# Performance work log

Measured on AMD Instinct MI355X. Metric: run time of the kernel, lower is better.

Reference implementation:

```python
import jax, jax.numpy as jnp
import numpy as np

B, C, H, W = 8, 96, 224, 224
WS, SS, NH = 7, 3, 3          # window size, shift size, num heads
HD = C // NH                  # head dim = 32
N = WS * WS                   # tokens per window = 49
MLP_H = 4 * C
EPS = 1e-5


def _rel_pos_index():
    coords = np.stack(np.meshgrid(np.arange(WS), np.arange(WS), indexing='ij'))  # (2, ws, ws)
    cf = coords.reshape(2, -1)                       # (2, N)
    rel = cf[:, :, None] - cf[:, None, :]            # (2, N, N)
    rel = rel.transpose(1, 2, 0).copy()              # (N, N, 2)
    rel[:, :, 0] += WS - 1
    rel[:, :, 1] += WS - 1
    rel[:, :, 0] *= 2 * WS - 1
    return rel.sum(-1)                               # (N, N) int


def _attn_mask():
    # Swin shifted-window mask: (num_windows, N, N) with 0 / -100
    img = np.zeros((H, W), np.float32)
    cnt = 0
    for hs in (slice(0, -WS), slice(-WS, -SS), slice(-SS, None)):
        for ws_ in (slice(0, -WS), slice(-WS, -SS), slice(-SS, None)):
            img[hs, ws_] = cnt
            cnt += 1
    mw = img.reshape(H // WS, WS, W // WS, WS).transpose(0, 2, 1, 3).reshape(-1, N)
    m = mw[:, None, :] - mw[:, :, None]
    return np.where(m != 0, np.float32(-100.0), np.float32(0.0))


def setup_inputs() -> dict:
    key = jax.random.key(0)
    ks = jax.random.split(key, 8)
    s = 0.02
    return {
        "x": jax.random.normal(ks[0], (B, C, H, W), jnp.float32),
        "attn_mask": jnp.asarray(_attn_mask()),
        "norm1_g": jnp.ones((C,), jnp.float32),
        "norm1_b": jnp.zeros((C,), jnp.float32),
        "qkv_w": jax.random.normal(ks[1], (C, 3 * C), jnp.float32) * s,
        "qkv_b": jnp.zeros((3 * C,), jnp.float32),
        "rpb": jax.random.normal(ks[2], ((2 * WS - 1) ** 2, NH), jnp.float32) * s,
        "proj_w": jax.random.normal(ks[3], (C, C), jnp.float32) * s,
        "proj_b": jnp.zeros((C,), jnp.float32),
        "norm2_g": jnp.ones((C,), jnp.float32),
        "norm2_b": jnp.zeros((C,), jnp.float32),
        "fc1_w": jax.random.normal(ks[4], (C, MLP_H), jnp.float32) * s,
        "fc1_b": jnp.zeros((MLP_H,), jnp.float32),
        "fc2_w": jax.random.normal(ks[5], (MLP_H, C), jnp.float32) * s,
        "fc2_b": jnp.zeros((C,), jnp.float32),
    }


def _ln(x, g, b):
    mu = jnp.mean(x, axis=-1, keepdims=True)
    var = jnp.var(x, axis=-1, keepdims=True)
    return (x - mu) * jax.lax.rsqrt(var + EPS) * g + b


def reference(x, attn_mask, norm1_g, norm1_b, qkv_w, qkv_b, rpb, proj_w, proj_b,
              norm2_g, norm2_b, fc1_w, fc1_b, fc2_w, fc2_b):
    shortcut = x
    # (B,C,H,W) -> (B,HW,C) -> LN -> (B,H,W,C)
    xl = jnp.transpose(x, (0, 2, 3, 1)).reshape(B, H * W, C)
    xl = _ln(xl, norm1_g, norm1_b).reshape(B, H, W, C)
    # H,W divisible by WS: pad_r = pad_b = 0
    sx = jnp.roll(xl, (-SS, -SS), axis=(1, 2))
    # window partition -> (B*nW, N, C)
    xw = sx.reshape(B, H // WS, WS, W // WS, WS, C).transpose(0, 1, 3, 2, 4, 5).reshape(-1, N, C)
    B_ = xw.shape[0]
    nW = B_ // B
    qkv = (xw @ qkv_w + qkv_b).reshape(B_, N, 3, NH, HD).transpose(2, 0, 3, 1, 4)
    q = qkv[0] * (HD ** -0.5)
    k, v = qkv[1], qkv[2]
    attn = jnp.einsum('bhnd,bhmd->bhnm', q, k)           # (B_, NH, N, N)
    rel_idx = jnp.asarray(_rel_pos_index())
    bias = rpb[rel_idx.reshape(-1)].reshape(N, N, NH).transpose(2, 0, 1)  # (NH, N, N)
    attn = attn + bias[None]
    attn = attn.reshape(B, nW, NH, N, N) + attn_mask[None, :, None]
    attn = jax.nn.softmax(attn.reshape(B_, NH, N, N), axis=-1)
    out = jnp.einsum('bhnm,bhmd->bhnd', attn, v).transpose(0, 2, 1, 3).reshape(B_, N, C)
    out = out @ proj_w + proj_b
    # window reverse -> (B, H, W, C)
    out = out.reshape(B, H // WS, W // WS, WS, WS, C).transpose(0, 1, 3, 2, 4, 5).reshape(B, H, W, C)
    out = jnp.roll(out, (SS, SS), axis=(1, 2))
    # faithful to original: permute(0,1,3,2) then raw reshape to (B,C,H,W)
    out = jnp.transpose(out, (0, 1, 3, 2)).reshape(B, C, H, W)
    x1 = shortcut + out
    # MLP branch, faithful: permute(0,1,3,2) then raw reshape to (B,HW,C)
    xm = jnp.transpose(x1, (0, 1, 3, 2)).reshape(B, H * W, C)
    xm = _ln(xm, norm2_g, norm2_b)
    xm = jax.nn.gelu(xm @ fc1_w + fc1_b, approximate=False) @ fc2_w + fc2_b
    xm = xm.reshape(B, C, H, W)
    return x1 + xm
```

## Files before the change

kernel.cpp:

```cpp
#include <hip/hip_runtime.h>
#include <hip/hip_bf16.h>


typedef __attribute__((ext_vector_type(4))) float f32x4;
typedef __attribute__((ext_vector_type(8))) short s16x8;

constexpr int B_ = 8;
constexpr int M_ = 96 * 224 * 224;

__device__ __forceinline__ ushort f2bs(float f) {
    __hip_bfloat16 h = __float2bfloat16(f);
    ushort u; __builtin_memcpy(&u, &h, 2); return u;
}
__device__ __forceinline__ float bs2f(ushort u) {
    __hip_bfloat16 h; __builtin_memcpy(&h, &u, 2); return __bfloat162float(h);
}
__device__ __forceinline__ f32x4 mfma16(s16x8 a, s16x8 b, f32x4 c) {
    return __builtin_amdgcn_mfma_f32_16x16x32_bf16(a, b, c, 0, 0, 0);
}
__device__ __forceinline__ float gelu_f(float v) {
    float s  = v * 0.70710678118654752f;
    float as = fabsf(s);
    float t  = __builtin_amdgcn_rcpf(fmaf(0.3275911f, as, 1.0f));
    float p  = fmaf(fmaf(fmaf(fmaf(1.061405429f, t, -1.453152027f), t,
                   1.421413741f), t, -0.284496736f), t, 0.254829592f) * t;
    float y  = 1.0f - p * __expf(-s * s);
    float er = copysignf(y, s);
    return 0.5f * v * (1.0f + er);
}

__global__ __launch_bounds__(256) void prep_kernel(
    const float* __restrict__ qkvw, const float* __restrict__ projw,
    const float* __restrict__ w1,   const float* __restrict__ w2,
    ushort* __restrict__ wq, ushort* __restrict__ wp,
    ushort* __restrict__ wf1, ushort* __restrict__ wf2)
{
    int i = blockIdx.x * 256 + threadIdx.x;
    if (i < 27648) { int n = i / 96, k = i % 96;  wq[i]  = f2bs(qkvw[k * 288 + n]); }
    if (i < 9216)  { int n = i / 96, k = i % 96;  wp[i]  = f2bs(projw[k * 96 + n]); }
    if (i < 36864) {
        int n = i / 96,  k = i % 96;   wf1[i] = f2bs(w1[k * 384 + n]);
        int n2 = i / 384, k2 = i % 384; wf2[i] = f2bs(w2[k2 * 96 + n2]);
    }
}

__global__ __launch_bounds__(256) void attn_kernel(
    const float* __restrict__ x,
    const float* __restrict__ amask,
    const float* __restrict__ n1g, const float* __restrict__ n1b,
    const float* __restrict__ qkvb,
    const float* __restrict__ rpb,
    const float* __restrict__ projb,
    const ushort* __restrict__ wq, const ushort* __restrict__ wp,
    ushort* __restrict__ x1)
{
    __shared__ __align__(16) ushort T[64][104];
    __shared__ __align__(16) ushort K[64][104];
    __shared__ __align__(16) ushort vT[96][72];
    __shared__ __align__(16) ushort Pws[4][16][72];
    __shared__ float rpbs[512];

    const int tid  = threadIdx.x;
    const int wave = tid >> 6, lane = tid & 63;
    const int cu   = lane & 15;
    const int g4   = lane >> 4;
    const int gk8  = g4 << 3;
    const int gr4  = g4 << 2;

    const int blk = (blockIdx.x & 7) * 1024 + (blockIdx.x >> 3);
    const int b   = blk >> 10;
    const int wi  = blk & 1023;
    const int wh  = wi >> 5, ww = wi & 31;
    const int bM  = b * M_;
    const bool need_mask = (wh == 31) || (ww == 31);

    for (int i = tid; i < 507; i += 256) rpbs[i] = rpb[i];

    const int t49 = tid % 49;
    const int g5  = tid / 49;
    int hh_s = 0, wc_s = 0;
    if (tid < 245) {
        int i = t49 / 7, j = t49 % 7;
        hh_s = wh * 7 + i + 3; if (hh_s >= 224) hh_s -= 224;
        wc_s = ww * 7 + j + 3; if (wc_s >= 224) wc_s -= 224;
    }

    if (tid < 245) {
        const float* xp = x + bM + g5 * 50176 + hh_s * 224 + wc_s;
        ushort* dT = &T[t49][g5];
        for (int c = g5; c < 96; c += 5) {
            *dT = f2bs(*xp);
            xp += 5 * 50176; dT += 5;
        }
    }
    {
        uint* z = (uint*)&T[49][0];
        for (int i = tid; i < 780; i += 256) z[i] = 0u;
    }
    __syncthreads();

    if (tid < 196) {
        int t = tid >> 2, s = tid & 3;
        float sum = 0.f, sq = 0.f;
        float vv[24];
        #pragma unroll
        for (int i = 0; i < 24; ++i) {
            vv[i] = bs2f(T[t][s * 24 + i]);
            sum += vv[i]; sq += vv[i] * vv[i];
        }
        sum += __shfl_xor(sum, 1); sq += __shfl_xor(sq, 1);
        sum += __shfl_xor(sum, 2); sq += __shfl_xor(sq, 2);
        float mu   = sum * (1.0f / 96.0f);
        float rstd = rsqrtf(sq * (1.0f / 96.0f) - mu * mu + 1e-5f);
        #pragma unroll
        for (int i = 0; i < 24; ++i) {
            int c = s * 24 + i;
            T[t][c] = f2bs((vv[i] - mu) * rstd * n1g[c] + n1b[c]);
        }
    }
    __syncthreads();

    const int ar = (wave << 4) | cu;
    const int tr = (wave << 4) + gr4;

    {
        s16x8 a0 = *(const s16x8*)&T[ar][gk8];
        s16x8 a1 = *(const s16x8*)&T[ar][32 + gk8];
        s16x8 a2 = *(const s16x8*)&T[ar][64 + gk8];
        f32x4 qreg[6];
        #pragma unroll
        for (int nt = 0; nt < 18; ++nt) {
            int nc = (nt << 4) | cu;
            const ushort* bp = wq + nc * 96 + gk8;
            s16x8 b0 = *(const s16x8*)(bp);
            s16x8 b1 = *(const s16x8*)(bp + 32);
            s16x8 b2 = *(const s16x8*)(bp + 64);
            f32x4 acc = {0.f, 0.f, 0.f, 0.f};
            acc = mfma16(a0, b0, acc);
            acc = mfma16(a1, b1, acc);
            acc = mfma16(a2, b2, acc);
            float bias = qkvb[nc];
            if (nt < 6) {
                #pragma unroll
                for (int r = 0; r < 4; ++r)
                    qreg[nt][r] = (acc[r] + bias) * 0.17677669529663689f;
            } else if (nc < 192) {
                #pragma unroll
                for (int r = 0; r < 4; ++r) K[tr + r][nc - 96] = f2bs(acc[r] + bias);
            } else {
                int d = nc - 192;
                ushort4 pk;
                pk.x = f2bs(acc[0] + bias); pk.y = f2bs(acc[1] + bias);
                pk.z = f2bs(acc[2] + bias); pk.w = f2bs(acc[3] + bias);
                *(ushort4*)&vT[d][tr] = pk;
            }
        }
        #pragma unroll
        for (int qn = 0; qn < 6; ++qn)
            #pragma unroll
            for (int r = 0; r < 4; ++r)
                T[tr + r][(qn << 4) | cu] = f2bs(qreg[qn][r]);
    }
    __syncthreads();

    int u7d[4], u7m[4];
    #pragma unroll
    for (int ut = 0; ut < 4; ++ut) {
        int u = (ut << 4) | cu;
        u7d[ut] = u / 7; u7m[ut] = u % 7;
    }
    s16x8 ones8;
    #pragma unroll
    for (int i = 0; i < 8; ++i) ones8[i] = (short)0x3F80;

    #pragma unroll
    for (int it = 0; it < 3; ++it) {
        const int hh = it;
        const int t0r = tr;

        s16x8 aq = *(const s16x8*)&T[ar][(hh << 5) + gk8];
        f32x4 sa[4];
        #pragma unroll
        for (int ut = 0; ut < 4; ++ut) {
            s16x8 bk = *(const s16x8*)&K[(ut << 4) | cu][(hh << 5) + gk8];
            f32x4 z = {0.f, 0.f, 0.f, 0.f};
            sa[ut] = mfma16(aq, bk, z);
        }
        #pragma unroll
        for (int ut = 0; ut < 4; ++ut) {
            int u = (ut << 4) | cu;
            #pragma unroll
            for (int r = 0; r < 4; ++r) {
                int t = t0r + r;
                float s = sa[ut][r];
                if (t < 49 && u < 49) {
                    int dr = t / 7 - u7d[ut] + 6, dc = t % 7 - u7m[ut] + 6;
                    s += rpbs[(dr * 13 + dc) * 3 + hh];
                    if (need_mask) s += amask[(wi * 49 + t) * 49 + u];
                } else if (u >= 49) {
                    s = -1e30f;
                }
                sa[ut][r] = s;
            }
        }
        #pragma unroll
        for (int r = 0; r < 4; ++r) {
            float m = fmaxf(fmaxf(sa[0][r], sa[1][r]), fmaxf(sa[2][r], sa[3][r]));
            m = fmaxf(m, __shfl_xor(m, 1)); m = fmaxf(m, __shfl_xor(m, 2));
            m = fmaxf(m, __shfl_xor(m, 4)); m = fmaxf(m, __shfl_xor(m, 8));
            sa[0][r] = __expf(sa[0][r] - m);
            sa[1][r] = __expf(sa[1][r] - m);
            sa[2][r] = __expf(sa[2][r] - m);
            sa[3][r] = __expf(sa[3][r] - m);
        }
        #pragma unroll
        for (int ut = 0; ut < 4; ++ut) {
            int u = (ut << 4) | cu;
            #pragma unroll
            for (int r = 0; r < 4; ++r) Pws[wave][gr4 + r][u] = f2bs(sa[ut][r]);
        }
        s16x8 pa0 = *(const s16x8*)&Pws[wave][cu][gk8];
        s16x8 pa1 = *(const s16x8*)&Pws[wave][cu][32 + gk8];
        f32x4 accd = {0.f, 0.f, 0.f, 0.f};
        accd = mfma16(pa0, ones8, accd);
        accd = mfma16(pa1, ones8, accd);
        f32x4 acco[2];
        #pragma unroll
        for (int nt = 0; nt < 2; ++nt) {
            int d = (hh << 5) + (nt << 4) + cu;
            s16x8 bv0 = *(const s16x8*)&vT[d][gk8];
            s16x8 bv1 = *(const s16x8*)&vT[d][32 + gk8];
            f32x4 acc = {0.f, 0.f, 0.f, 0.f};
            acc = mfma16(pa0, bv0, acc);
            acc = mfma16(pa1, bv1, acc);
            acco[nt] = acc;
        }
        float inv[4];
        #pragma unroll
        for (int r = 0; r < 4; ++r) inv[r] = __builtin_amdgcn_rcpf(accd[r]);
        #pragma unroll
        for (int nt = 0; nt < 2; ++nt)
            #pragma unroll
            for (int r = 0; r < 4; ++r)
                T[t0r + r][(hh << 5) + (nt << 4) + cu] = f2bs(acco[nt][r] * inv[r]);
    }

    {
        s16x8 a0 = *(const s16x8*)&T[ar][gk8];
        s16x8 a1 = *(const s16x8*)&T[ar][32 + gk8];
        s16x8 a2 = *(const s16x8*)&T[ar][64 + gk8];
        #pragma unroll
        for (int nt = 0; nt < 6; ++nt) {
            int nc = (nt << 4) | cu;
            const ushort* bp = wp + nc * 96 + gk8;
            s16x8 b0 = *(const s16x8*)(bp);
            s16x8 b1 = *(const s16x8*)(bp + 32);
            s16x8 b2 = *(const s16x8*)(bp + 64);
            f32x4 acc = {0.f, 0.f, 0.f, 0.f};
            acc = mfma16(a0, b0, acc);
            acc = mfma16(a1, b1, acc);
            acc = mfma16(a2, b2, acc);
            float bias = projb[nc];
            #pragma unroll
            for (int r = 0; r < 4; ++r) T[tr + r][nc] = f2bs(acc[r] + bias);
        }
    }
    __syncthreads();

    if (tid < 245) {
        const int base = bM + (hh_s * 96 + g5) * 224 + wc_s;
        const float* xp = x + base;
        ushort* dx = x1 + base;
        const ushort* Tp = &T[t49][g5];
        for (int c = g5; c < 96; c += 5) {
            *dx = f2bs(*xp + bs2f(*Tp));
            xp += 5 * 224; dx += 5 * 224; Tp += 5;
        }
    }
}

__global__ __launch_bounds__(256) void transpose_kernel(
    const ushort* __restrict__ x1, ushort* __restrict__ x1p)
{
    __shared__ ushort tile[32][36];
    const int id      = blockIdx.x;
    const int tile_id = id % 49;
    const int slab    = id / 49;
    const int h0 = (tile_id / 7) * 32;
    const int w0 = (tile_id % 7) * 32;
    const ushort* src = x1  + slab * 50176;
    ushort*       dst = x1p + slab * 50176;

    const int i = threadIdx.x >> 3;
    const int j = (threadIdx.x & 7) * 4;

    *(ushort4*)&tile[i][j] = *(const ushort4*)&src[(h0 + i) * 224 + w0 + j];
    __syncthreads();
    ushort4 v;
    v.x = tile[j][i]; v.y = tile[j + 1][i]; v.z = tile[j + 2][i]; v.w = tile[j + 3][i];
    *(ushort4*)&dst[(w0 + i) * 224 + h0 + j] = v;
}

template <bool CLEAN>
__device__ __forceinline__ void ln_token(
    const ushort* __restrict__ xsrc, int tok, int gk8,
    const float* __restrict__ n2g, const float* __restrict__ n2b,
    s16x8& a0, s16x8& a1, s16x8& a2)
{
    float vals[24];
    if (CLEAN) {
        const ushort* base = xsrc + tok * 96 + gk8;
        s16x8 r0 = *(const s16x8*)(base);
        s16x8 r1 = *(const s16x8*)(base + 32);
        s16x8 r2 = *(const s16x8*)(base + 64);
        #pragma unroll
        for (int i = 0; i < 8; ++i) {
            vals[i]      = bs2f((ushort)r0[i]);
            vals[8 + i]  = bs2f((ushort)r1[i]);
            vals[16 + i] = bs2f((ushort)r2[i]);
        }
    } else {
        int bb = tok / 50176;
        int tl = tok % 50176;
        #pragma unroll
        for (int s = 0; s < 3; ++s)
            #pragma unroll
            for (int i = 0; i < 8; ++i) {
                int p = tl * 96 + gk8 + s * 32 + i;
                int c = p / 50176, rem = p % 50176;
                int w = rem / 224, h = rem % 224;
                vals[s * 8 + i] = bs2f(xsrc[bb * M_ + c * 50176 + h * 224 + w]);
            }
    }
    float sum = 0.f, sq = 0.f;
    #pragma unroll
    for (int i = 0; i < 24; ++i) { sum += vals[i]; sq += vals[i] * vals[i]; }
    sum += __shfl_xor(sum, 16); sq += __shfl_xor(sq, 16);
    sum += __shfl_xor(sum, 32); sq += __shfl_xor(sq, 32);
    float mu   = sum * (1.0f / 96.0f);
    float rstd = rsqrtf(sq * (1.0f / 96.0f) - mu * mu + 1e-5f);
    #pragma unroll
    for (int i = 0; i < 8; ++i) {
        int c0 = gk8 + i, c1 = gk8 + 32 + i, c2 = gk8 + 64 + i;
        a0[i] = (short)f2bs((vals[i]      - mu) * rstd * n2g[c0] + n2b[c0]);
        a1[i] = (short)f2bs((vals[8 + i]  - mu) * rstd * n2g[c1] + n2b[c1]);
        a2[i] = (short)f2bs((vals[16 + i] - mu) * rstd * n2g[c2] + n2b[c2]);
    }
}

template <bool CLEAN>
__global__ __launch_bounds__(256) void mlp_kernel(
    const ushort* __restrict__ xsrc,
    const ushort* __restrict__ x1flat,
    const float* __restrict__ n2g, const float* __restrict__ n2b,
    const float* __restrict__ b1v, const float* __restrict__ b2v,
    const ushort* __restrict__ wf1, const ushort* __restrict__ wf2,
    float* __restrict__ out)
{
    __shared__ __align__(16) ushort hS[4][2][32][40];

    const int tid  = threadIdx.x;
    const int wave = tid >> 6, lane = tid & 63;
    const int cu   = lane & 15;
    const int g4   = lane >> 4;
    const int gk8  = g4 << 3;
    const int gr4  = g4 << 2;
    const int t0g  = blockIdx.x * 128;
    const int tokA = t0g + (wave << 5) + cu;
    const int tokB = tokA + 16;

    s16x8 aA0, aA1, aA2, aB0, aB1, aB2;
    ln_token<CLEAN>(xsrc, tokA, gk8, n2g, n2b, aA0, aA1, aA2);
    ln_token<CLEAN>(xsrc, tokB, gk8, n2g, n2b, aB0, aB1, aB2);

    auto fc1_step = [&](int s, int buf) {
        #pragma unroll
        for (int half = 0; half < 2; ++half) {
            int nc = ((2 * s + half) << 4) | cu;
            const ushort* bp = wf1 + nc * 96 + gk8;
            s16x8 b0 = *(const s16x8*)(bp);
            s16x8 b1 = *(const s16x8*)(bp + 32);
            s16x8 b2 = *(const s16x8*)(bp + 64);
            float bias = b1v[nc];
            f32x4 accA = {0.f, 0.f, 0.f, 0.f};
            accA = mfma16(aA0, b0, accA);
            accA = mfma16(aA1, b1, accA);
            accA = mfma16(aA2, b2, accA);
            f32x4 accB = {0.f, 0.f, 0.f, 0.f};
            accB = mfma16(aB0, b0, accB);
            accB = mfma16(aB1, b1, accB);
            accB = mfma16(aB2, b2, accB);
            #pragma unroll
            for (int r = 0; r < 4; ++r) {
                hS[wave][buf][gr4 + r][(half << 4) | cu]      = f2bs(gelu_f(accA[r] + bias));
                hS[wave][buf][16 + gr4 + r][(half << 4) | cu] = f2bs(gelu_f(accB[r] + bias));
            }
        }
    };

    f32x4 oaccA[6], oaccB[6];
    #pragma unroll
    for (int nt2 = 0; nt2 < 6; ++nt2) {
        oaccA[nt2] = (f32x4){0.f, 0.f, 0.f, 0.f};
        oaccB[nt2] = (f32x4){0.f, 0.f, 0.f, 0.f};
    }

    fc1_step(0, 0);
    for (int s = 0; s < 12; ++s) {
        int buf = s & 1;
        s16x8 haA = *(const s16x8*)&hS[wave][buf][cu][gk8];
        s16x8 haB = *(const s16x8*)&hS[wave][buf][16 + cu][gk8];
        if (s < 11) fc1_step(s + 1, buf ^ 1);
        #pragma unroll
        for (int nt2 = 0; nt2 < 6; ++nt2) {
            int nc2 = (nt2 << 4) | cu;
            s16x8 bv = *(const s16x8*)&wf2[nc2 * 384 + s * 32 + gk8];
            oaccA[nt2] = mfma16(haA, bv, oaccA[nt2]);
            oaccB[nt2] = mfma16(haB, bv, oaccB[nt2]);
        }
    }

    const int trow = (wave << 5) + gr4;
    #pragma unroll
    for (int nt2 = 0; nt2 < 6; ++nt2) {
        int nc2 = (nt2 << 4) | cu;
        float bias = b2v[nc2];
        #pragma unroll
        for (int r = 0; r < 4; ++r) {
            int GA = (t0g + trow + r) * 96 + nc2;
            out[GA] = bias + oaccA[nt2][r] + bs2f(x1flat[GA]);
            int GB = GA + 16 * 96;
            out[GB] = bias + oaccB[nt2][r] + bs2f(x1flat[GB]);
        }
    }
}

extern "C" void kernel_launch(void* const* d_in, const int* in_sizes, int n_in,
                              void* d_out, int out_size, void* d_ws, size_t ws_size,
                              hipStream_t stream) {
    const float* x      = (const float*)d_in[0];
    const float* amask  = (const float*)d_in[1];
    const float* n1g    = (const float*)d_in[2];
    const float* n1b    = (const float*)d_in[3];
    const float* qkvw   = (const float*)d_in[4];
    const float* qkvb   = (const float*)d_in[5];
    const float* rpb    = (const float*)d_in[6];
    const float* projw  = (const float*)d_in[7];
    const float* projb  = (const float*)d_in[8];
    const float* n2g    = (const float*)d_in[9];
    const float* n2b    = (const float*)d_in[10];
    const float* w1     = (const float*)d_in[11];
    const float* b1     = (const float*)d_in[12];
    const float* w2     = (const float*)d_in[13];
    const float* b2     = (const float*)d_in[14];

    char* ws = (char*)d_ws;
    ushort* wq  = (ushort*)(ws);
    ushort* wp  = (ushort*)(ws + 55296);
    ushort* wf1 = (ushort*)(ws + 73728);
    ushort* wf2 = (ushort*)(ws + 147456);
    ushort* x1  = (ushort*)(ws + 262144);
    ushort* x1p = (ushort*)(ws + 77332480);
    float* out = (float*)d_out;

    const bool clean = (ws_size >= (size_t)154402816);

    prep_kernel<<<dim3(144), dim3(256), 0, stream>>>(qkvw, projw, w1, w2, wq, wp, wf1, wf2);

    attn_kernel<<<dim3(8192), dim3(256), 0, stream>>>(
        x, amask, n1g, n1b, qkvb, rpb, projb, wq, wp, x1);

    if (clean) {
        transpose_kernel<<<dim3(37632), dim3(256), 0, stream>>>(x1, x1p);
        mlp_kernel<true><<<dim3(3136), dim3(256), 0, stream>>>(
            x1p, x1, n2g, n2b, b1, b2, wf1, wf2, out);
    } else {
        mlp_kernel<false><<<dim3(3136), dim3(256), 0, stream>>>(
            x1, x1, n2g, n2b, b1, b2, wf1, wf2, out);
    }
}
```

Measured before the change: 641.1 us.

## Double attention block to 512 threads, splitting QKV, heads and projection across waves

The attention kernel now runs 8 waves per window instead of 4. The QKV GEMM columns are split between two wave halves, the three heads are shared unevenly (waves 0-3 take heads 0 and 2, waves 4-7 take head 1), and the output projection columns are split in half. The goal is more parallelism per window, which should shorten the serial MFMA chains and spread the gather and scatter over more threads. To avoid read/write hazards the T buffer is widened, and one extra barrier is added. The head split leaves the work imbalanced, and the larger block raises LDS use, which may reduce occupancy.

```diff
diff --git a/kernel.cpp b/kernel.cpp
--- a/kernel.cpp
+++ b/kernel.cpp
@@ -44,7 +44,7 @@
     }
 }
 
-__global__ __launch_bounds__(256) void attn_kernel(
+__global__ __launch_bounds__(512) void attn_kernel(
     const float* __restrict__ x,
     const float* __restrict__ amask,
     const float* __restrict__ n1g, const float* __restrict__ n1b,
@@ -54,10 +54,10 @@
     const ushort* __restrict__ wq, const ushort* __restrict__ wp,
     ushort* __restrict__ x1)
 {
-    __shared__ __align__(16) ushort T[64][104];
+    __shared__ __align__(16) ushort T[64][200];
     __shared__ __align__(16) ushort K[64][104];
     __shared__ __align__(16) ushort vT[96][72];
-    __shared__ __align__(16) ushort Pws[4][16][72];
+    __shared__ __align__(16) ushort Pws[8][16][72];
     __shared__ float rpbs[512];
 
     const int tid  = threadIdx.x;
@@ -74,92 +74,114 @@
     const int bM  = b * M_;
     const bool need_mask = (wh == 31) || (ww == 31);
 
-    for (int i = tid; i < 507; i += 256) rpbs[i] = rpb[i];
+    for (int i = tid; i < 507; i += 512) rpbs[i] = rpb[i];
 
     const int t49 = tid % 49;
-    const int g5  = tid / 49;
+    const int g10 = tid / 49;
     int hh_s = 0, wc_s = 0;
-    if (tid < 245) {
+    if (tid < 490) {
         int i = t49 / 7, j = t49 % 7;
         hh_s = wh * 7 + i + 3; if (hh_s >= 224) hh_s -= 224;
         wc_s = ww * 7 + j + 3; if (wc_s >= 224) wc_s -= 224;
     }
 
-    if (tid < 245) {
-        const float* xp = x + bM + g5 * 50176 + hh_s * 224 + wc_s;
-        ushort* dT = &T[t49][g5];
-        for (int c = g5; c < 96; c += 5) {
+    if (tid < 490) {
+        const float* xp = x + bM + g10 * 50176 + hh_s * 224 + wc_s;
+        ushort* dT = &T[t49][g10];
+        for (int c = g10; c < 96; c += 10) {
             *dT = f2bs(*xp);
-            xp += 5 * 50176; dT += 5;
-        }
-    }
-    {
-        uint* z = (uint*)&T[49][0];
-        for (int i = tid; i < 780; i += 256) z[i] = 0u;
+            xp += 10 * 50176; dT += 10;
+        }
+    }
+    for (int idx = tid; idx < 15 * 48; idx += 512) {
+        int row = 49 + idx / 48, col = idx % 48;
+        ((uint*)&T[0][0])[row * 100 + col] = 0u;
     }
     __syncthreads();
 
-    if (tid < 196) {
-        int t = tid >> 2, s = tid & 3;
+    if (tid < 392) {
+        int t = tid >> 3, s = tid & 7;
         float sum = 0.f, sq = 0.f;
-        float vv[24];
-        #pragma unroll
-        for (int i = 0; i < 24; ++i) {
-            vv[i] = bs2f(T[t][s * 24 + i]);
+        float vv[12];
+        #pragma unroll
+        for (int i = 0; i < 12; ++i) {
+            vv[i] = bs2f(T[t][s * 12 + i]);
             sum += vv[i]; sq += vv[i] * vv[i];
         }
         sum += __shfl_xor(sum, 1); sq += __shfl_xor(sq, 1);
         sum += __shfl_xor(sum, 2); sq += __shfl_xor(sq, 2);
+        sum += __shfl_xor(sum, 4); sq += __shfl_xor(sq, 4);
         float mu   = sum * (1.0f / 96.0f);
         float rstd = rsqrtf(sq * (1.0f / 96.0f) - mu * mu + 1e-5f);
         #pragma unroll
-        for (int i = 0; i < 24; ++i) {
-            int c = s * 24 + i;
+        for (int i = 0; i < 12; ++i) {
+            int c = s * 12 + i;
             T[t][c] = f2bs((vv[i] - mu) * rstd * n1g[c] + n1b[c]);
         }
     }
     __syncthreads();
 
-    const int ar = (wave << 4) | cu;
-    const int tr = (wave << 4) + gr4;
+    const int mt = wave & 3, nh = wave >> 2;
+    const int ar = (mt << 4) | cu;
+    const int tr = (mt << 4) + gr4;
 
     {
         s16x8 a0 = *(const s16x8*)&T[ar][gk8];
         s16x8 a1 = *(const s16x8*)&T[ar][32 + gk8];
         s16x8 a2 = *(const s16x8*)&T[ar][64 + gk8];
-        f32x4 qreg[6];
-        #pragma unroll
-        for (int nt = 0; nt < 18; ++nt) {
-            int nc = (nt << 4) | cu;
-            const ushort* bp = wq + nc * 96 + gk8;
-            s16x8 b0 = *(const s16x8*)(bp);
-            s16x8 b1 = *(const s16x8*)(bp + 32);
-            s16x8 b2 = *(const s16x8*)(bp + 64);
-            f32x4 acc = {0.f, 0.f, 0.f, 0.f};
-            acc = mfma16(a0, b0, acc);
-            acc = mfma16(a1, b1, acc);
-            acc = mfma16(a2, b2, acc);
-            float bias = qkvb[nc];
-            if (nt < 6) {
+        if (nh == 0) {
+            f32x4 qreg[6];
+            #pragma unroll
+            for (int k = 0; k < 9; ++k) {
+                int nc = (k << 4) | cu;
+                const ushort* bp = wq + nc * 96 + gk8;
+                s16x8 b0 = *(const s16x8*)(bp);
+                s16x8 b1 = *(const s16x8*)(bp + 32);
+                s16x8 b2 = *(const s16x8*)(bp + 64);
+                f32x4 acc = {0.f, 0.f, 0.f, 0.f};
+                acc = mfma16(a0, b0, acc);
+                acc = mfma16(a1, b1, acc);
+                acc = mfma16(a2, b2, acc);
+                float bias = qkvb[nc];
+                if (k < 6) {
+                    #pragma unroll
+                    for (int r = 0; r < 4; ++r)
+                        qreg[k][r] = (acc[r] + bias) * 0.17677669529663689f;
+                } else {
+                    #pragma unroll
+                    for (int r = 0; r < 4; ++r) K[tr + r][nc - 96] = f2bs(acc[r] + bias);
+                }
+            }
+            #pragma unroll
+            for (int qn = 0; qn < 6; ++qn)
                 #pragma unroll
                 for (int r = 0; r < 4; ++r)
-                    qreg[nt][r] = (acc[r] + bias) * 0.17677669529663689f;
-            } else if (nc < 192) {
-                #pragma unroll
-                for (int r = 0; r < 4; ++r) K[tr + r][nc - 96] = f2bs(acc[r] + bias);
-            } else {
-                int d = nc - 192;
-                ushort4 pk;
-                pk.x = f2bs(acc[0] + bias); pk.y = f2bs(acc[1] + bias);
-                pk.z = f2bs(acc[2] + bias); pk.w = f2bs(acc[3] + bias);
-                *(ushort4*)&vT[d][tr] = pk;
+                    T[tr + r][96 + ((qn << 4) | cu)] = f2bs(qreg[qn][r]);
+        } else {
+            #pragma unroll
+            for (int k = 0; k < 9; ++k) {
+                int nc = ((9 + k) << 4) | cu;
+                const ushort* bp = wq + nc * 96 + gk8;
+                s16x8 b0 = *(const s16x8*)(bp);
+                s16x8 b1 = *(const s16x8*)(bp + 32);
+                s16x8 b2 = *(const s16x8*)(bp + 64);
+                f32x4 acc = {0.f, 0.f, 0.f, 0.f};
+                acc = mfma16(a0, b0, acc);
+                acc = mfma16(a1, b1, acc);
+                acc = mfma16(a2, b2, acc);
+                float bias = qkvb[nc];
+                if (k < 3) {
+                    #pragma unroll
+                    for (int r = 0; r < 4; ++r) K[tr + r][nc - 96] = f2bs(acc[r] + bias);
+                } else {
+                    int d = nc - 192;
+                    ushort4 pk;
+                    pk.x = f2bs(acc[0] + bias); pk.y = f2bs(acc[1] + bias);
+                    pk.z = f2bs(acc[2] + bias); pk.w = f2bs(acc[3] + bias);
+                    *(ushort4*)&vT[d][tr] = pk;
+                }
             }
         }
-        #pragma unroll
-        for (int qn = 0; qn < 6; ++qn)
-            #pragma unroll
-            for (int r = 0; r < 4; ++r)
-                T[tr + r][(qn << 4) | cu] = f2bs(qreg[qn][r]);
     }
     __syncthreads();
 
@@ -173,12 +195,13 @@
     #pragma unroll
     for (int i = 0; i < 8; ++i) ones8[i] = (short)0x3F80;
 
-    #pragma unroll
-    for (int it = 0; it < 3; ++it) {
-        const int hh = it;
-        const int t0r = tr;
-
-        s16x8 aq = *(const s16x8*)&T[ar][(hh << 5) + gk8];
+    const int tt  = mt;
+    const int t0r = (tt << 4) + gr4;
+    const int nTask = (wave < 4) ? 2 : 1;
+    for (int it = 0; it < nTask; ++it) {
+        const int hh = (wave < 4) ? (it << 1) : 1;
+
+        s16x8 aq = *(const s16x8*)&T[(tt << 4) | cu][96 + (hh << 5) + gk8];
         f32x4 sa[4];
         #pragma unroll
         for (int ut = 0; ut < 4; ++ut) {
@@ -244,14 +267,15 @@
             for (int r = 0; r < 4; ++r)
                 T[t0r + r][(hh << 5) + (nt << 4) + cu] = f2bs(acco[nt][r] * inv[r]);
     }
+    __syncthreads();
 
     {
         s16x8 a0 = *(const s16x8*)&T[ar][gk8];
         s16x8 a1 = *(const s16x8*)&T[ar][32 + gk8];
         s16x8 a2 = *(const s16x8*)&T[ar][64 + gk8];
         #pragma unroll
-        for (int nt = 0; nt < 6; ++nt) {
-            int nc = (nt << 4) | cu;
+        for (int k = 0; k < 3; ++k) {
+            int nc = ((3 * nh + k) << 4) | cu;
             const ushort* bp = wp + nc * 96 + gk8;
             s16x8 b0 = *(const s16x8*)(bp);
             s16x8 b1 = *(const s16x8*)(bp + 32);
@@ -262,19 +286,19 @@
             acc = mfma16(a2, b2, acc);
             float bias = projb[nc];
             #pragma unroll
-            for (int r = 0; r < 4; ++r) T[tr + r][nc] = f2bs(acc[r] + bias);
+            for (int r = 0; r < 4; ++r) T[tr + r][96 + nc] = f2bs(acc[r] + bias);
         }
     }
     __syncthreads();
 
-    if (tid < 245) {
-        const int base = bM + (hh_s * 96 + g5) * 224 + wc_s;
+    if (tid < 490) {
+        const int base = bM + (hh_s * 96 + g10) * 224 + wc_s;
         const float* xp = x + base;
         ushort* dx = x1 + base;
-        const ushort* Tp = &T[t49][g5];
-        for (int c = g5; c < 96; c += 5) {
+        const ushort* Tp = &T[t49][96 + g10];
+        for (int c = g10; c < 96; c += 10) {
             *dx = f2bs(*xp + bs2f(*Tp));
-            xp += 5 * 224; dx += 5 * 224; Tp += 5;
+            xp += 10 * 224; dx += 10 * 224; Tp += 10;
         }
     }
 }
@@ -467,7 +491,7 @@
 
     prep_kernel<<<dim3(144), dim3(256), 0, stream>>>(qkvw, projw, w1, w2, wq, wp, wf1, wf2);
 
-    attn_kernel<<<dim3(8192), dim3(256), 0, stream>>>(
+    attn_kernel<<<dim3(8192), dim3(512), 0, stream>>>(
         x, amask, n1g, n1b, qkvb, rpb, projb, wq, wp, x1);
 
     if (clean) {
```

New measurement: 695.3 us. 8.5% more time.
